# Kernel tuning notes

Hardware: AMD Instinct MI355X
Metric: run time of the kernel (lower is better)

The kernel has to match this reference:

```python
import jax, jax.numpy as jnp
import numpy as np

N, E, G = 50000, 600000, 512
F_IN, H, OUT = 128, 128, 256


def setup_inputs() -> dict:
    key = jax.random.key(0)
    ks = jax.random.split(key, 16)
    x = jax.random.normal(ks[0], (N, F_IN), dtype=jnp.float32)
    edge_index = jax.random.randint(ks[1], (2, E), 0, N, dtype=jnp.int64)
    batch = jnp.sort(jax.random.randint(ks[2], (N,), 0, G, dtype=jnp.int64))
    def lin(k, out_d, in_d):
        s = 1.0 / np.sqrt(in_d)
        return jax.random.uniform(k, (out_d, in_d), jnp.float32, -s, s)
    W1l, W1r = lin(ks[3], H, F_IN), lin(ks[4], H, F_IN)
    b1 = jnp.zeros((H,), jnp.float32)
    W2l, W2r = lin(ks[5], H, H), lin(ks[6], H, H)
    b2 = jnp.zeros((H,), jnp.float32)
    W3l, W3r = lin(ks[7], H, H), lin(ks[8], H, H)
    b3 = jnp.zeros((H,), jnp.float32)
    Wlin = lin(ks[9], OUT, 2 * H)
    blin = jnp.zeros((OUT,), jnp.float32)
    return dict(x=x, edge_index=edge_index, batch=batch,
                W1l=W1l, b1=b1, W1r=W1r, W2l=W2l, b2=b2, W2r=W2r,
                W3l=W3l, b3=b3, W3r=W3r, Wlin=Wlin, blin=blin)


def reference(x, edge_index, batch, W1l, b1, W1r, W2l, b2, W2r, W3l, b3, W3r, Wlin, blin):
    src, dst = edge_index[0], edge_index[1]
    # in-degree of each target node (mean aggregation denominator)
    deg = jax.ops.segment_sum(jnp.ones((E,), x.dtype), dst, num_segments=N)
    deg = jnp.maximum(deg, 1.0)[:, None]

    def sage(h, Wl, bl, Wr):
        # mean-aggregate neighbor features then linear; plus root transform
        agg = jax.ops.segment_sum(h[src], dst, num_segments=N) / deg
        return agg @ Wl.T + bl + h @ Wr.T

    h = jax.nn.relu(sage(x, W1l, b1, W1r))
    h = jax.nn.relu(sage(h, W2l, b2, W2r))
    h = sage(h, W3l, b3, W3r)

    # global max / mean pool per graph
    x_max = jax.ops.segment_max(h, batch, num_segments=G)
    x_max = jnp.where(jnp.isfinite(x_max), x_max, 0.0)
    cnt = jnp.maximum(jax.ops.segment_sum(jnp.ones((N,), h.dtype), batch, num_segments=G), 1.0)
    x_mean = jax.ops.segment_sum(h, batch, num_segments=G) / cnt[:, None]

    pooled = jnp.concatenate([x_max, x_mean], axis=1)  # [G, 2H]
    # dropout is identity in eval mode
    return pooled @ Wlin.T + blin
```

## Files before the change

### kernel.cpp

```cpp
#include <hip/hip_runtime.h>
#include <hip/hip_bf16.h>
#include <hip/hip_fp16.h>


#define FH 128
#define OUTD 256
#define SCHUNK 2048

typedef unsigned int u32;
typedef unsigned short u16;
typedef __attribute__((ext_vector_type(8))) _Float16 f16frag;
typedef __attribute__((ext_vector_type(4))) float f4frag;

typedef __attribute__((address_space(3))) u32 lds_u32;
typedef __attribute__((address_space(1))) const u32 glb_u32;

__device__ inline void async_copy16(const void* g, void* l) {
    __builtin_amdgcn_global_load_lds((glb_u32*)g, (lds_u32*)l, 16, 0, 0);
}

__global__ void prep_all(const float* __restrict__ x, u16* __restrict__ x16, int n4, int PX,
                         const float* __restrict__ W0, const float* __restrict__ W1,
                         const float* __restrict__ W2, const float* __restrict__ W3,
                         const float* __restrict__ W4, const float* __restrict__ W5,
                         uint4* __restrict__ Bf, int PW,
                         const int* __restrict__ dst, int* __restrict__ cnt, int E) {
    int blk = blockIdx.x;
    if (blk < PX) {
        int id = blk * 256 + threadIdx.x;
        if (id >= n4) return;
        float4 v = *(const float4*)(x + (size_t)id * 4);
        __half h0 = __float2half(v.x), h1 = __float2half(v.y);
        __half h2 = __float2half(v.z), h3 = __float2half(v.w);
        ushort4 s;
        s.x = *(u16*)&h0; s.y = *(u16*)&h1; s.z = *(u16*)&h2; s.w = *(u16*)&h3;
        *(ushort4*)(x16 + (size_t)id * 4) = s;
    } else if (blk < PX + PW) {
        int pair = (blk - PX) * 4 + (threadIdx.x >> 6);
        if (pair >= 48) return;
        int ks = pair & 7;
        int arr = pair >> 3;
        int l = threadIdx.x & 63;
        const float* Ws[6] = {W0, W1, W2, W3, W4, W5};
        const float* W = Ws[arr];
        bool use_lo = (ks >= 4);
        int kb = (ks & 3) * 32 + (l >> 4) * 8;
        uint4* out = Bf + (size_t)arr * 4096;
        #pragma unroll
        for (int ot = 0; ot < 8; ++ot) {
            int o = ot * 16 + (l & 15);
            u32 h[8];
            #pragma unroll
            for (int i = 0; i < 8; ++i) {
                float v = W[o * 128 + kb + i];
                __half hi = __float2half(v);
                if (use_lo) {
                    float rem = v - __half2float(hi);
                    __half lo = __float2half(rem);
                    h[i] = *(u16*)&lo;
                } else {
                    h[i] = *(u16*)&hi;
                }
            }
            uint4 u;
            u.x = h[0] | (h[1] << 16);
            u.y = h[2] | (h[3] << 16);
            u.z = h[4] | (h[5] << 16);
            u.w = h[6] | (h[7] << 16);
            out[(ks * 8 + ot) * 64 + l] = u;
        }
    } else {
        int e = (blk - PX - PW) * 256 + threadIdx.x;
        if (e < E) atomicAdd(&cnt[dst[e]], 1);
    }
}

__global__ void scanA_kernel(const int* __restrict__ cnt, int* __restrict__ bsum, int n) {
    __shared__ int ws[4];
    int b = blockIdx.x, t = threadIdx.x;
    int base = b * SCHUNK + t * 8;
    int s = 0;
    #pragma unroll
    for (int k = 0; k < 8; ++k) {
        int i = base + k;
        s += (i < n) ? cnt[i] : 0;
    }
    #pragma unroll
    for (int off = 32; off >= 1; off >>= 1) s += __shfl_xor(s, off, 64);
    int w = t >> 6, lane = t & 63;
    if (lane == 0) ws[w] = s;
    __syncthreads();
    if (t == 0) bsum[b] = ws[0] + ws[1] + ws[2] + ws[3];
}

__global__ void scanC_kernel(const int* __restrict__ cnt, const int* __restrict__ bsum,
                             int NB, int* __restrict__ rp, float* __restrict__ dinv, int n) {
    __shared__ int ws[4];
    __shared__ int base_s;
    int b = blockIdx.x, t = threadIdx.x;
    if (t < 64) {
        int v = (t < NB) ? bsum[t] : 0;
        int pre = (t < b) ? v : 0;
        #pragma unroll
        for (int off = 32; off >= 1; off >>= 1) pre += __shfl_xor(pre, off, 64);
        if (t == 0) base_s = pre;
        if (b == 0) {
            int tot = v;
            #pragma unroll
            for (int off = 32; off >= 1; off >>= 1) tot += __shfl_xor(tot, off, 64);
            if (t == 0) rp[n] = tot;
        }
    }
    __syncthreads();
    int boff = base_s;
    int base = b * SCHUNK + t * 8;
    int v[8];
    int ts = 0;
    #pragma unroll
    for (int k = 0; k < 8; ++k) {
        int i = base + k;
        v[k] = (i < n) ? cnt[i] : 0;
        ts += v[k];
    }
    int w = t >> 6, lane = t & 63;
    int x = ts;
    #pragma unroll
    for (int off = 1; off < 64; off <<= 1) {
        int y = __shfl_up(x, off, 64);
        if (lane >= off) x += y;
    }
    if (lane == 63) ws[w] = x;
    __syncthreads();
    int woff = 0;
    #pragma unroll
    for (int q = 0; q < 4; ++q) woff += (q < w) ? ws[q] : 0;
    int run = boff + woff + (x - ts);
    #pragma unroll
    for (int k = 0; k < 8; ++k) {
        int i = base + k;
        if (i < n) {
            rp[i] = run;
            dinv[i] = 1.0f / (float)max(v[k], 1);
        }
        run += v[k];
    }
}

__global__ void scatter_bounds(const int* __restrict__ src, const int* __restrict__ dst,
                               const int* __restrict__ rp, int* __restrict__ cursor,
                               int* __restrict__ esrc, int E, int SC,
                               const int* __restrict__ batch, int* __restrict__ gstart,
                               int n, int g) {
    int blk = blockIdx.x;
    if (blk < SC) {
        int e = blk * 256 + threadIdx.x;
        if (e < E) {
            int d = dst[e];
            int pos = rp[d] + atomicAdd(&cursor[d], 1);
            esrc[pos] = src[e];
        }
    } else {
        int i = (blk - SC) * 256 + threadIdx.x;
        if (i >= n) return;
        int b = batch[i];
        int pb = (i == 0) ? -1 : batch[i - 1];
        for (int q = pb + 1; q <= b; ++q) gstart[q] = i;
        if (i == n - 1) {
            for (int q = b + 1; q <= g; ++q) gstart[q] = n;
        }
    }
}

__device__ inline void add8(float* a, uint4 u) {
    float2 f0 = __half22float2(*(__half2*)&u.x);
    float2 f1 = __half22float2(*(__half2*)&u.y);
    float2 f2 = __half22float2(*(__half2*)&u.z);
    float2 f3 = __half22float2(*(__half2*)&u.w);
    a[0] += f0.x; a[1] += f0.y; a[2] += f1.x; a[3] += f1.y;
    a[4] += f2.x; a[5] += f2.y; a[6] += f3.x; a[7] += f3.y;
}

__global__ void agg_kernel(const u16* __restrict__ h16,
                           const int* __restrict__ rp, const int* __restrict__ esrc,
                           const float* __restrict__ dinv,
                           u16* __restrict__ agg16, int n_nodes) {
    int node = blockIdx.x * 16 + (threadIdx.x >> 4);
    if (node >= n_nodes) return;
    int lane = threadIdx.x & 15;
    int f = lane * 8;
    int s0 = rp[node], s1 = rp[node + 1];
    float a0[8] = {0, 0, 0, 0, 0, 0, 0, 0};
    float a1[8] = {0, 0, 0, 0, 0, 0, 0, 0};
    float a2[8] = {0, 0, 0, 0, 0, 0, 0, 0};
    float a3[8] = {0, 0, 0, 0, 0, 0, 0, 0};
    int j = s0;
    for (; j + 8 <= s1; j += 8) {
        int i0 = esrc[j],     i1 = esrc[j + 1], i2 = esrc[j + 2], i3 = esrc[j + 3];
        int i4 = esrc[j + 4], i5 = esrc[j + 5], i6 = esrc[j + 6], i7 = esrc[j + 7];
        uint4 u0 = *(const uint4*)(h16 + (size_t)i0 * FH + f);
        uint4 u1 = *(const uint4*)(h16 + (size_t)i1 * FH + f);
        uint4 u2 = *(const uint4*)(h16 + (size_t)i2 * FH + f);
        uint4 u3 = *(const uint4*)(h16 + (size_t)i3 * FH + f);
        uint4 u4 = *(const uint4*)(h16 + (size_t)i4 * FH + f);
        uint4 u5 = *(const uint4*)(h16 + (size_t)i5 * FH + f);
        uint4 u6 = *(const uint4*)(h16 + (size_t)i6 * FH + f);
        uint4 u7 = *(const uint4*)(h16 + (size_t)i7 * FH + f);
        add8(a0, u0); add8(a1, u1); add8(a2, u2); add8(a3, u3);
        add8(a0, u4); add8(a1, u5); add8(a2, u6); add8(a3, u7);
    }
    if (j + 4 <= s1) {
        int i0 = esrc[j], i1 = esrc[j + 1], i2 = esrc[j + 2], i3 = esrc[j + 3];
        uint4 u0 = *(const uint4*)(h16 + (size_t)i0 * FH + f);
        uint4 u1 = *(const uint4*)(h16 + (size_t)i1 * FH + f);
        uint4 u2 = *(const uint4*)(h16 + (size_t)i2 * FH + f);
        uint4 u3 = *(const uint4*)(h16 + (size_t)i3 * FH + f);
        add8(a0, u0); add8(a1, u1); add8(a2, u2); add8(a3, u3);
        j += 4;
    }
    for (; j < s1; ++j) {
        uint4 u0 = *(const uint4*)(h16 + (size_t)esrc[j] * FH + f);
        add8(a0, u0);
    }
    float di = dinv[node];
    u32 oh[8];
    #pragma unroll
    for (int i = 0; i < 8; ++i) {
        __half hv = __float2half((a0[i] + a1[i] + a2[i] + a3[i]) * di);
        oh[i] = *(u16*)&hv;
    }
    uint4 w;
    w.x = oh[0] | (oh[1] << 16);
    w.y = oh[2] | (oh[3] << 16);
    w.z = oh[4] | (oh[5] << 16);
    w.w = oh[6] | (oh[7] << 16);
    *(uint4*)(agg16 + (size_t)node * FH + f) = w;
}

__global__ __launch_bounds__(256, 2)
void mfma_gemm(const u16* __restrict__ A1, const u16* __restrict__ A2,
               const uint4* __restrict__ Bf1, const uint4* __restrict__ Bf2,
               const float* __restrict__ bias, u16* __restrict__ out16,
               int do_relu) {
    __shared__ uint4 Bl[4096];
    int tid = threadIdx.x;
    int l = tid & 63;
    int wv = tid >> 6;
    int bn0 = blockIdx.x * 192 + wv * 48;
    int m = l & 15, q = l >> 4;

    f4frag acc[3][8];
    #pragma unroll
    for (int i = 0; i < 3; ++i)
        #pragma unroll
        for (int o = 0; o < 8; ++o)
            acc[i][o] = (f4frag){0.f, 0.f, 0.f, 0.f};

    #pragma unroll
    for (int p = 0; p < 2; ++p) {
        const u16* P = p ? A2 : A1;
        const uint4* Bf = p ? Bf2 : Bf1;

        f16frag Af[3][4];
        #pragma unroll
        for (int nt = 0; nt < 3; ++nt)
            #pragma unroll
            for (int s = 0; s < 4; ++s)
                Af[nt][s] = *(const f16frag*)(P + (size_t)(bn0 + nt * 16 + m) * FH + s * 32 + q * 8);

        __syncthreads();

        #pragma unroll
        for (int u = 0; u < 16; ++u)
            async_copy16(Bf + (size_t)u * 256 + wv * 64 + l,
                         &Bl[u * 256 + wv * 64]);
        __syncthreads();

        #pragma unroll
        for (int s = 0; s < 4; ++s) {
            {
                f16frag B[8];
                #pragma unroll
                for (int ot = 0; ot < 8; ++ot)
                    B[ot] = *(const f16frag*)&Bl[(size_t)(s * 8 + ot) * 64 + l];
                #pragma unroll
                for (int ot = 0; ot < 8; ++ot)
                    #pragma unroll
                    for (int nt = 0; nt < 3; ++nt)
                        acc[nt][ot] = __builtin_amdgcn_mfma_f32_16x16x32_f16(Af[nt][s], B[ot], acc[nt][ot], 0, 0, 0);
            }
            {
                f16frag B[8];
                #pragma unroll
                for (int ot = 0; ot < 8; ++ot)
                    B[ot] = *(const f16frag*)&Bl[(size_t)((s + 4) * 8 + ot) * 64 + l];
                #pragma unroll
                for (int ot = 0; ot < 8; ++ot)
                    #pragma unroll
                    for (int nt = 0; nt < 3; ++nt)
                        acc[nt][ot] = __builtin_amdgcn_mfma_f32_16x16x32_f16(Af[nt][s], B[ot], acc[nt][ot], 0, 0, 0);
            }
        }
    }

    #pragma unroll
    for (int nt = 0; nt < 3; ++nt)
        #pragma unroll
        for (int r = 0; r < 4; ++r) {
            int node = bn0 + nt * 16 + q * 4 + r;
            #pragma unroll
            for (int ot = 0; ot < 8; ++ot) {
                float v = acc[nt][ot][r] + bias[ot * 16 + m];
                if (do_relu) v = fmaxf(v, 0.f);
                __half hv = __float2half(v);
                out16[(size_t)node * FH + ot * 16 + m] = *(u16*)&hv;
            }
        }
}

__global__ __launch_bounds__(256, 2)
void pool_final(const u16* __restrict__ h16, const int* __restrict__ gstart,
                const float* __restrict__ Wlin, const float* __restrict__ blin,
                float* __restrict__ out) {
    __shared__ float smax[16][FH];
    __shared__ float ssum[16][FH];
    __shared__ float pr[2 * FH];
    int g = blockIdx.x;
    int tid = threadIdx.x;
    int way = tid >> 4;
    int lane = tid & 15;
    int f = lane * 8;
    int s = gstart[g], e = gstart[g + 1];

    float mx[8], sm[8];
    #pragma unroll
    for (int i = 0; i < 8; ++i) { mx[i] = -INFINITY; sm[i] = 0.f; }
    for (int n = s + way; n < e; n += 16) {
        uint4 u = *(const uint4*)(h16 + (size_t)n * FH + f);
        float2 f0 = __half22float2(*(__half2*)&u.x);
        float2 f1 = __half22float2(*(__half2*)&u.y);
        float2 f2 = __half22float2(*(__half2*)&u.z);
        float2 f3 = __half22float2(*(__half2*)&u.w);
        float v[8] = {f0.x, f0.y, f1.x, f1.y, f2.x, f2.y, f3.x, f3.y};
        #pragma unroll
        for (int i = 0; i < 8; ++i) {
            mx[i] = fmaxf(mx[i], v[i]);
            sm[i] += v[i];
        }
    }
    #pragma unroll
    for (int i = 0; i < 8; ++i) {
        smax[way][f + i] = mx[i];
        ssum[way][f + i] = sm[i];
    }
    __syncthreads();
    int c = e - s;
    if (tid < FH) {
        float m2 = -INFINITY, s2 = 0.f;
        #pragma unroll
        for (int w2 = 0; w2 < 16; ++w2) {
            m2 = fmaxf(m2, smax[w2][tid]);
            s2 += ssum[w2][tid];
        }
        pr[tid] = (c > 0) ? m2 : 0.f;
        pr[FH + tid] = s2 / (float)max(c, 1);
    }
    __syncthreads();
    int o = tid;
    const float4* wr = (const float4*)(Wlin + (size_t)o * (2 * FH));
    float acc = 0.f;
    #pragma unroll
    for (int j = 0; j < (2 * FH) / 4; ++j) {
        float4 wv = wr[j];
        acc += wv.x * pr[j * 4 + 0] + wv.y * pr[j * 4 + 1] +
               wv.z * pr[j * 4 + 2] + wv.w * pr[j * 4 + 3];
    }
    out[(size_t)g * OUTD + o] = acc + blin[o];
}

extern "C" void kernel_launch(void* const* d_in, const int* in_sizes, int n_in,
                              void* d_out, int out_size, void* d_ws, size_t ws_size,
                              hipStream_t stream) {
    const float* x     = (const float*)d_in[0];
    const int*   ei    = (const int*)d_in[1];
    const int*   batch = (const int*)d_in[2];
    const float* W1l = (const float*)d_in[3];
    const float* b1  = (const float*)d_in[4];
    const float* W1r = (const float*)d_in[5];
    const float* W2l = (const float*)d_in[6];
    const float* b2  = (const float*)d_in[7];
    const float* W2r = (const float*)d_in[8];
    const float* W3l = (const float*)d_in[9];
    const float* b3  = (const float*)d_in[10];
    const float* W3r = (const float*)d_in[11];
    const float* Wlin = (const float*)d_in[12];
    const float* blin = (const float*)d_in[13];
    float* out = (float*)d_out;

    const int E = in_sizes[1] / 2;
    const int N = in_sizes[2];
    const int G = out_size / OUTD;
    const int* src = ei;
    const int* dst = ei + E;
    const int NB = (N + SCHUNK - 1) / SCHUNK;
    const int GB = (N + 191) / 192;
    const int NP = GB * 192;

    char* w = (char*)d_ws;
    auto alloc = [&](size_t bytes) {
        void* p = (void*)w;
        w += (bytes + 255) & ~(size_t)255;
        return p;
    };
    int*   cnt    = (int*)alloc((size_t)2 * N * sizeof(int));
    int*   cursor = cnt + N;
    int*   rp     = (int*)alloc((size_t)(N + 1) * sizeof(int));
    int*   esrc   = (int*)alloc((size_t)E * sizeof(int));
    int*   gstart = (int*)alloc((size_t)(G + 1) * sizeof(int));
    float* dinv   = (float*)alloc((size_t)N * sizeof(float));
    int*   bsum   = (int*)alloc(64 * sizeof(int));
    u16*   x16    = (u16*)alloc((size_t)NP * FH * sizeof(u16));
    u16*   agg16  = (u16*)alloc((size_t)NP * FH * sizeof(u16));
    u16*   hA16   = (u16*)alloc((size_t)NP * FH * sizeof(u16));
    u16*   hB16   = (u16*)alloc((size_t)NP * FH * sizeof(u16));
    uint4* BF     = (uint4*)alloc((size_t)6 * 4096 * sizeof(uint4));
    (void)ws_size;

    hipMemsetAsync(cnt, 0, (size_t)2 * N * sizeof(int), stream);
    const int n4 = N * 32;
    const int PX = (n4 + 255) / 256;
    const int PW = 12;
    const int PH = (E + 255) / 256;
    prep_all<<<PX + PW + PH, 256, 0, stream>>>(x, x16, n4, PX,
                                               W1l, W1r, W2l, W2r, W3l, W3r, BF, PW,
                                               dst, cnt, E);

    scanA_kernel<<<NB, 256, 0, stream>>>(cnt, bsum, N);
    scanC_kernel<<<NB, 256, 0, stream>>>(cnt, bsum, NB, rp, dinv, N);
    const int SC = (E + 255) / 256;
    const int GBND = (N + 255) / 256;
    scatter_bounds<<<SC + GBND, 256, 0, stream>>>(src, dst, rp, cursor, esrc, E, SC,
                                                  batch, gstart, N, G);

    const int agg_grid = (N + 15) / 16;

    agg_kernel<<<agg_grid, 256, 0, stream>>>(x16, rp, esrc, dinv, agg16, N);
    mfma_gemm<<<GB, 256, 0, stream>>>(agg16, x16, BF + 0 * 4096, BF + 1 * 4096, b1, hA16, 1);
    agg_kernel<<<agg_grid, 256, 0, stream>>>(hA16, rp, esrc, dinv, agg16, N);
    mfma_gemm<<<GB, 256, 0, stream>>>(agg16, hA16, BF + 2 * 4096, BF + 3 * 4096, b2, hB16, 1);
    agg_kernel<<<agg_grid, 256, 0, stream>>>(hB16, rp, esrc, dinv, agg16, N);
    mfma_gemm<<<GB, 256, 0, stream>>>(agg16, hB16, BF + 4 * 4096, BF + 5 * 4096, b3, hA16, 0);

    pool_final<<<G, 256, 0, stream>>>(hA16, gstart, Wlin, blin, out);
}
```

Before: 323.8 us.

## Fuse neighbor mean aggregation into the SAGE MFMA GEMM kernel

Removes the separate aggregation kernel and intermediate agg buffer. Each GEMM wave gathers and averages neighbour features directly into its A-fragment registers before running the MFMA products against the two weight matrices, loading the first weight tile asynchronously during the gather. This eliminates a round trip of the aggregated tensor through global memory and three kernel launches. In exchange it greatly reduces the number of threads doing latency-bound gathers and introduces per-row degree divergence inside waves.

```diff
diff --git a/kernel.cpp b/kernel.cpp
--- a/kernel.cpp
+++ b/kernel.cpp
@@ -180,73 +180,79 @@
     a[4] += f2.x; a[5] += f2.y; a[6] += f3.x; a[7] += f3.y;
 }
 
-__global__ void agg_kernel(const u16* __restrict__ h16,
-                           const int* __restrict__ rp, const int* __restrict__ esrc,
-                           const float* __restrict__ dinv,
-                           u16* __restrict__ agg16, int n_nodes) {
-    int node = blockIdx.x * 16 + (threadIdx.x >> 4);
-    if (node >= n_nodes) return;
-    int lane = threadIdx.x & 15;
-    int f = lane * 8;
-    int s0 = rp[node], s1 = rp[node + 1];
-    float a0[8] = {0, 0, 0, 0, 0, 0, 0, 0};
-    float a1[8] = {0, 0, 0, 0, 0, 0, 0, 0};
-    float a2[8] = {0, 0, 0, 0, 0, 0, 0, 0};
-    float a3[8] = {0, 0, 0, 0, 0, 0, 0, 0};
-    int j = s0;
-    for (; j + 8 <= s1; j += 8) {
-        int i0 = esrc[j],     i1 = esrc[j + 1], i2 = esrc[j + 2], i3 = esrc[j + 3];
-        int i4 = esrc[j + 4], i5 = esrc[j + 5], i6 = esrc[j + 6], i7 = esrc[j + 7];
-        uint4 u0 = *(const uint4*)(h16 + (size_t)i0 * FH + f);
-        uint4 u1 = *(const uint4*)(h16 + (size_t)i1 * FH + f);
-        uint4 u2 = *(const uint4*)(h16 + (size_t)i2 * FH + f);
-        uint4 u3 = *(const uint4*)(h16 + (size_t)i3 * FH + f);
-        uint4 u4 = *(const uint4*)(h16 + (size_t)i4 * FH + f);
-        uint4 u5 = *(const uint4*)(h16 + (size_t)i5 * FH + f);
-        uint4 u6 = *(const uint4*)(h16 + (size_t)i6 * FH + f);
-        uint4 u7 = *(const uint4*)(h16 + (size_t)i7 * FH + f);
-        add8(a0, u0); add8(a1, u1); add8(a2, u2); add8(a3, u3);
-        add8(a0, u4); add8(a1, u5); add8(a2, u6); add8(a3, u7);
-    }
-    if (j + 4 <= s1) {
-        int i0 = esrc[j], i1 = esrc[j + 1], i2 = esrc[j + 2], i3 = esrc[j + 3];
-        uint4 u0 = *(const uint4*)(h16 + (size_t)i0 * FH + f);
-        uint4 u1 = *(const uint4*)(h16 + (size_t)i1 * FH + f);
-        uint4 u2 = *(const uint4*)(h16 + (size_t)i2 * FH + f);
-        uint4 u3 = *(const uint4*)(h16 + (size_t)i3 * FH + f);
-        add8(a0, u0); add8(a1, u1); add8(a2, u2); add8(a3, u3);
-        j += 4;
-    }
-    for (; j < s1; ++j) {
-        uint4 u0 = *(const uint4*)(h16 + (size_t)esrc[j] * FH + f);
-        add8(a0, u0);
-    }
-    float di = dinv[node];
-    u32 oh[8];
-    #pragma unroll
-    for (int i = 0; i < 8; ++i) {
-        __half hv = __float2half((a0[i] + a1[i] + a2[i] + a3[i]) * di);
-        oh[i] = *(u16*)&hv;
-    }
-    uint4 w;
-    w.x = oh[0] | (oh[1] << 16);
-    w.y = oh[2] | (oh[3] << 16);
-    w.z = oh[4] | (oh[5] << 16);
-    w.w = oh[6] | (oh[7] << 16);
-    *(uint4*)(agg16 + (size_t)node * FH + f) = w;
-}
-
 __global__ __launch_bounds__(256, 2)
-void mfma_gemm(const u16* __restrict__ A1, const u16* __restrict__ A2,
-               const uint4* __restrict__ Bf1, const uint4* __restrict__ Bf2,
-               const float* __restrict__ bias, u16* __restrict__ out16,
-               int do_relu) {
+void sage_layer(const u16* __restrict__ h16,
+                const int* __restrict__ rp, const int* __restrict__ esrc,
+                const float* __restrict__ dinv,
+                const uint4* __restrict__ Bf1, const uint4* __restrict__ Bf2,
+                const float* __restrict__ bias, u16* __restrict__ out16,
+                int n_nodes, int do_relu) {
     __shared__ uint4 Bl[4096];
     int tid = threadIdx.x;
     int l = tid & 63;
     int wv = tid >> 6;
     int bn0 = blockIdx.x * 192 + wv * 48;
     int m = l & 15, q = l >> 4;
+    int qb = q * 8;
+
+    #pragma unroll
+    for (int u = 0; u < 16; ++u)
+        async_copy16(Bf1 + (size_t)u * 256 + wv * 64 + l,
+                     &Bl[u * 256 + wv * 64]);
+    f16frag Af2[3][4];
+    #pragma unroll
+    for (int nt = 0; nt < 3; ++nt)
+        #pragma unroll
+        for (int s = 0; s < 4; ++s)
+            Af2[nt][s] = *(const f16frag*)(h16 + (size_t)(bn0 + nt * 16 + m) * FH + s * 32 + qb);
+
+    f16frag Af1[3][4];
+    #pragma unroll
+    for (int nt = 0; nt < 3; ++nt) {
+        int node = bn0 + nt * 16 + m;
+        float a[4][8];
+        #pragma unroll
+        for (int s = 0; s < 4; ++s)
+            #pragma unroll
+            for (int i = 0; i < 8; ++i) a[s][i] = 0.f;
+        int s0 = 0, s1 = 0;
+        if (node < n_nodes) { s0 = rp[node]; s1 = rp[node + 1]; }
+        int j = s0;
+        for (; j + 2 <= s1; j += 2) {
+            int i0 = esrc[j], i1 = esrc[j + 1];
+            const u16* p0 = h16 + (size_t)i0 * FH + qb;
+            const u16* p1 = h16 + (size_t)i1 * FH + qb;
+            uint4 u0[4], u1[4];
+            #pragma unroll
+            for (int s = 0; s < 4; ++s) {
+                u0[s] = *(const uint4*)(p0 + s * 32);
+                u1[s] = *(const uint4*)(p1 + s * 32);
+            }
+            #pragma unroll
+            for (int s = 0; s < 4; ++s) { add8(a[s], u0[s]); add8(a[s], u1[s]); }
+        }
+        if (j < s1) {
+            const u16* p0 = h16 + (size_t)esrc[j] * FH + qb;
+            #pragma unroll
+            for (int s = 0; s < 4; ++s) {
+                uint4 u0 = *(const uint4*)(p0 + s * 32);
+                add8(a[s], u0);
+            }
+        }
+        float di = (node < n_nodes) ? dinv[node] : 0.f;
+        #pragma unroll
+        for (int s = 0; s < 4; ++s) {
+            u32 oh[4];
+            #pragma unroll
+            for (int i = 0; i < 4; ++i) {
+                __half h0 = __float2half(a[s][2 * i] * di);
+                __half h1 = __float2half(a[s][2 * i + 1] * di);
+                oh[i] = (u32)(*(u16*)&h0) | ((u32)(*(u16*)&h1) << 16);
+            }
+            uint4 u; u.x = oh[0]; u.y = oh[1]; u.z = oh[2]; u.w = oh[3];
+            Af1[nt][s] = *(f16frag*)&u;
+        }
+    }
 
     f4frag acc[3][8];
     #pragma unroll
@@ -255,50 +261,64 @@
         for (int o = 0; o < 8; ++o)
             acc[i][o] = (f4frag){0.f, 0.f, 0.f, 0.f};
 
-    #pragma unroll
-    for (int p = 0; p < 2; ++p) {
-        const u16* P = p ? A2 : A1;
-        const uint4* Bf = p ? Bf2 : Bf1;
-
-        f16frag Af[3][4];
-        #pragma unroll
-        for (int nt = 0; nt < 3; ++nt)
-            #pragma unroll
-            for (int s = 0; s < 4; ++s)
-                Af[nt][s] = *(const f16frag*)(P + (size_t)(bn0 + nt * 16 + m) * FH + s * 32 + q * 8);
-
-        __syncthreads();
-
-        #pragma unroll
-        for (int u = 0; u < 16; ++u)
-            async_copy16(Bf + (size_t)u * 256 + wv * 64 + l,
-                         &Bl[u * 256 + wv * 64]);
-        __syncthreads();
-
-        #pragma unroll
-        for (int s = 0; s < 4; ++s) {
-            {
-                f16frag B[8];
+    __syncthreads();
+
+    #pragma unroll
+    for (int s = 0; s < 4; ++s) {
+        {
+            f16frag B[8];
+            #pragma unroll
+            for (int ot = 0; ot < 8; ++ot)
+                B[ot] = *(const f16frag*)&Bl[(size_t)(s * 8 + ot) * 64 + l];
+            #pragma unroll
+            for (int ot = 0; ot < 8; ++ot)
                 #pragma unroll
-                for (int ot = 0; ot < 8; ++ot)
-                    B[ot] = *(const f16frag*)&Bl[(size_t)(s * 8 + ot) * 64 + l];
+                for (int nt = 0; nt < 3; ++nt)
+                    acc[nt][ot] = __builtin_amdgcn_mfma_f32_16x16x32_f16(Af1[nt][s], B[ot], acc[nt][ot], 0, 0, 0);
+        }
+        {
+            f16frag B[8];
+            #pragma unroll
+            for (int ot = 0; ot < 8; ++ot)
+                B[ot] = *(const f16frag*)&Bl[(size_t)((s + 4) * 8 + ot) * 64 + l];
+            #pragma unroll
+            for (int ot = 0; ot < 8; ++ot)
                 #pragma unroll
-                for (int ot = 0; ot < 8; ++ot)
-                    #pragma unroll
-                    for (int nt = 0; nt < 3; ++nt)
-                        acc[nt][ot] = __builtin_amdgcn_mfma_f32_16x16x32_f16(Af[nt][s], B[ot], acc[nt][ot], 0, 0, 0);
-            }
-            {
-                f16frag B[8];
+                for (int nt = 0; nt < 3; ++nt)
+                    acc[nt][ot] = __builtin_amdgcn_mfma_f32_16x16x32_f16(Af1[nt][s], B[ot], acc[nt][ot], 0, 0, 0);
+        }
+    }
+
+    __syncthreads();
+    #pragma unroll
+    for (int u = 0; u < 16; ++u)
+        async_copy16(Bf2 + (size_t)u * 256 + wv * 64 + l,
+                     &Bl[u * 256 + wv * 64]);
+    __syncthreads();
+
+    #pragma unroll
+    for (int s = 0; s < 4; ++s) {
+        {
+            f16frag B[8];
+            #pragma unroll
+            for (int ot = 0; ot < 8; ++ot)
+                B[ot] = *(const f16frag*)&Bl[(size_t)(s * 8 + ot) * 64 + l];
+            #pragma unroll
+            for (int ot = 0; ot < 8; ++ot)
                 #pragma unroll
-                for (int ot = 0; ot < 8; ++ot)
-                    B[ot] = *(const f16frag*)&Bl[(size_t)((s + 4) * 8 + ot) * 64 + l];
+                for (int nt = 0; nt < 3; ++nt)
+                    acc[nt][ot] = __builtin_amdgcn_mfma_f32_16x16x32_f16(Af2[nt][s], B[ot], acc[nt][ot], 0, 0, 0);
+        }
+        {
+            f16frag B[8];
+            #pragma unroll
+            for (int ot = 0; ot < 8; ++ot)
+                B[ot] = *(const f16frag*)&Bl[(size_t)((s + 4) * 8 + ot) * 64 + l];
+            #pragma unroll
+            for (int ot = 0; ot < 8; ++ot)
                 #pragma unroll
-                for (int ot = 0; ot < 8; ++ot)
-                    #pragma unroll
-                    for (int nt = 0; nt < 3; ++nt)
-                        acc[nt][ot] = __builtin_amdgcn_mfma_f32_16x16x32_f16(Af[nt][s], B[ot], acc[nt][ot], 0, 0, 0);
-            }
+                for (int nt = 0; nt < 3; ++nt)
+                    acc[nt][ot] = __builtin_amdgcn_mfma_f32_16x16x32_f16(Af2[nt][s], B[ot], acc[nt][ot], 0, 0, 0);
         }
     }
 
@@ -419,7 +439,6 @@
     float* dinv   = (float*)alloc((size_t)N * sizeof(float));
     int*   bsum   = (int*)alloc(64 * sizeof(int));
     u16*   x16    = (u16*)alloc((size_t)NP * FH * sizeof(u16));
-    u16*   agg16  = (u16*)alloc((size_t)NP * FH * sizeof(u16));
     u16*   hA16   = (u16*)alloc((size_t)NP * FH * sizeof(u16));
     u16*   hB16   = (u16*)alloc((size_t)NP * FH * sizeof(u16));
     uint4* BF     = (uint4*)alloc((size_t)6 * 4096 * sizeof(uint4));
@@ -441,14 +460,12 @@
     scatter_bounds<<<SC + GBND, 256, 0, stream>>>(src, dst, rp, cursor, esrc, E, SC,
                                                   batch, gstart, N, G);
 
-    const int agg_grid = (N + 15) / 16;
-
-    agg_kernel<<<agg_grid, 256, 0, stream>>>(x16, rp, esrc, dinv, agg16, N);
-    mfma_gemm<<<GB, 256, 0, stream>>>(agg16, x16, BF + 0 * 4096, BF + 1 * 4096, b1, hA16, 1);
-    agg_kernel<<<agg_grid, 256, 0, stream>>>(hA16, rp, esrc, dinv, agg16, N);
-    mfma_gemm<<<GB, 256, 0, stream>>>(agg16, hA16, BF + 2 * 4096, BF + 3 * 4096, b2, hB16, 1);
-    agg_kernel<<<agg_grid, 256, 0, stream>>>(hB16, rp, esrc, dinv, agg16, N);
-    mfma_gemm<<<GB, 256, 0, stream>>>(agg16, hB16, BF + 4 * 4096, BF + 5 * 4096, b3, hA16, 0);
+    sage_layer<<<GB, 256, 0, stream>>>(x16, rp, esrc, dinv,
+                                       BF + 0 * 4096, BF + 1 * 4096, b1, hA16, N, 1);
+    sage_layer<<<GB, 256, 0, stream>>>(hA16, rp, esrc, dinv,
+                                       BF + 2 * 4096, BF + 3 * 4096, b2, hB16, N, 1);
+    sage_layer<<<GB, 256, 0, stream>>>(hB16, rp, esrc, dinv,
+                                       BF + 4 * 4096, BF + 5 * 4096, b3, hA16, N, 0);
 
     pool_final<<<G, 256, 0, stream>>>(hA16, gstart, Wlin, blin, out);
 }
```

Result: slower. 373.9 us (+15.5%).
